# Kernel tuning notes

Measured on AMD Instinct MI355X. Metric: run time of the kernel, lower is better.

Reference implementation:

```python
import jax, jax.numpy as jnp
import numpy as np
from jax import lax

D_MODEL, D_INNER, D_STATE, DT_RANK, K = 96, 192, 16, 6, 4
B_, H_, W_ = 8, 64, 64

def setup_inputs() -> dict:
    key = jax.random.key(0)
    ks = jax.random.split(key, 12)
    return {
        "x": jax.random.normal(ks[0], (B_, H_, W_, D_MODEL), jnp.float32),
        "in_proj_w": jax.random.normal(ks[1], (2 * D_INNER, D_MODEL), jnp.float32) * 0.05,
        "conv_w": jax.random.normal(ks[2], (D_INNER, 1, 3, 3), jnp.float32) * 0.1,
        "conv_b": jax.random.normal(ks[3], (D_INNER,), jnp.float32) * 0.01,
        "x_proj_w": jax.random.normal(ks[4], (K, DT_RANK + 2 * D_STATE, D_INNER), jnp.float32) * 0.05,
        "dt_proj_w": jax.random.normal(ks[5], (K, D_INNER, DT_RANK), jnp.float32) * 0.1,
        "dt_proj_b": jax.random.normal(ks[6], (K, D_INNER), jnp.float32) * 0.1,
        "A_logs": jax.random.uniform(ks[7], (K * D_INNER, D_STATE), jnp.float32, 0.0, 2.0),
        "Ds": jnp.ones((K * D_INNER,), jnp.float32),
        "ln_g": jnp.ones((D_INNER,), jnp.float32),
        "ln_b": jnp.zeros((D_INNER,), jnp.float32),
        "out_proj_w": jax.random.normal(ks[8], (D_MODEL, D_INNER), jnp.float32) * 0.05,
    }

def _selective_scan(xs, delta, A, Bs, Cs, Dk):
    # xs/delta: (B,K,D,L); A: (K,D,N); Bs/Cs: (B,K,N,L); Dk: (K,D)
    u_t = xs.transpose(3, 0, 1, 2)      # (L,B,K,D)
    d_t = delta.transpose(3, 0, 1, 2)   # (L,B,K,D)
    B_t = Bs.transpose(3, 0, 1, 2)      # (L,B,K,N)
    C_t = Cs.transpose(3, 0, 1, 2)      # (L,B,K,N)
    b = xs.shape[0]
    h0 = jnp.zeros((b, K, D_INNER, D_STATE), xs.dtype)
    def step(h, inp):
        ul, dl, Bl, Cl = inp
        dA = jnp.exp(dl[..., None] * A)                 # (B,K,D,N)
        h = dA * h + (dl * ul)[..., None] * Bl[:, :, None, :]
        y = jnp.einsum('bkdn,bkn->bkd', h, Cl)
        return h, y
    _, ys = lax.scan(step, h0, (u_t, d_t, B_t, C_t))
    y = ys.transpose(1, 2, 3, 0)                         # (B,K,D,L)
    return y + xs * Dk[None, :, :, None]

def reference(x, in_proj_w, conv_w, conv_b, x_proj_w, dt_proj_w, dt_proj_b,
              A_logs, Ds, ln_g, ln_b, out_proj_w):
    B, H, W, C = x.shape
    L = H * W
    xz = jnp.einsum('bhwc,ec->bhwe', x, in_proj_w)       # (B,H,W,2*D_inner)
    xc, z = jnp.split(xz, 2, axis=-1)
    xc = xc.transpose(0, 3, 1, 2)                        # (B,D,H,W)
    xc = lax.conv_general_dilated(xc, conv_w, (1, 1), 'SAME',
                                  dimension_numbers=('NCHW', 'OIHW', 'NCHW'),
                                  feature_group_count=D_INNER)
    xa = jax.nn.silu(xc + conv_b[None, :, None, None])
    x_flat = xa.reshape(B, D_INNER, L)
    x_wh = xa.transpose(0, 1, 3, 2).reshape(B, D_INNER, L)
    x_hwwh = jnp.stack([x_flat, x_wh], axis=1)           # (B,2,D,L)
    xs = jnp.concatenate([x_hwwh, jnp.flip(x_hwwh, -1)], axis=1)  # (B,4,D,L)
    x_dbl = jnp.einsum('bkdl,kcd->bkcl', xs, x_proj_w)
    dts = x_dbl[:, :, :DT_RANK]
    Bs = x_dbl[:, :, DT_RANK:DT_RANK + D_STATE]
    Cs = x_dbl[:, :, DT_RANK + D_STATE:]
    dts = jnp.einsum('bkrl,kdr->bkdl', dts, dt_proj_w)
    delta = jax.nn.softplus(dts + dt_proj_b[None, :, :, None])
    A = -jnp.exp(A_logs).reshape(K, D_INNER, D_STATE)
    Dk = Ds.reshape(K, D_INNER)
    out_y = _selective_scan(xs, delta, A, Bs, Cs, Dk)    # (B,4,D,L)
    y1 = out_y[:, 0]
    inv = jnp.flip(out_y[:, 2:4], -1)
    y2 = inv[:, 0]
    y3 = out_y[:, 1].reshape(B, D_INNER, W, H).transpose(0, 1, 3, 2).reshape(B, D_INNER, L)
    y4 = inv[:, 1].reshape(B, D_INNER, W, H).transpose(0, 1, 3, 2).reshape(B, D_INNER, L)
    y = (y1 + y2 + y3 + y4).transpose(0, 2, 1).reshape(B, H, W, D_INNER)
    mu = y.mean(-1, keepdims=True)
    var = ((y - mu) ** 2).mean(-1, keepdims=True)
    y = (y - mu) * lax.rsqrt(var + 1e-5) * ln_g + ln_b
    y = y * jax.nn.silu(z)
    return jnp.einsum('bhwd,cd->bhwc', y, out_proj_w)
```

## Files before the change

kernel.cpp:

```cpp
#include <hip/hip_runtime.h>

#define B_  8
#define L_  4096
#define DI  192
#define LOG2E 1.44269504f
#define LN2F  0.69314718f

#if __has_builtin(__builtin_amdgcn_exp2f)
#define EXP2(x) __builtin_amdgcn_exp2f(x)
#else
#define EXP2(x) __expf((x)*LN2F)
#endif

__global__ __launch_bounds__(256) void k_inproj(
    const float* __restrict__ x, const float* __restrict__ w,
    float* __restrict__ xc, float* __restrict__ z)
{
  __shared__ float As[96*68];
  __shared__ float Ws[96*68];
  const int t  = threadIdx.x;
  const int m0 = blockIdx.x * 64;
  const int n0 = blockIdx.y * 64;
  for (int i = t; i < 64*24; i += 256) {
    const int row = i / 24, q = (i % 24) * 4;
    const float4 v = *(const float4*)&x[(size_t)(m0+row)*96 + q];
    As[(q+0)*68 + row] = v.x; As[(q+1)*68 + row] = v.y;
    As[(q+2)*68 + row] = v.z; As[(q+3)*68 + row] = v.w;
  }
  for (int i = t; i < 64*24; i += 256) {
    const int row = i / 24, q = (i % 24) * 4;
    const float4 v = *(const float4*)&w[(size_t)(n0+row)*96 + q];
    Ws[(q+0)*68 + row] = v.x; Ws[(q+1)*68 + row] = v.y;
    Ws[(q+2)*68 + row] = v.z; Ws[(q+3)*68 + row] = v.w;
  }
  __syncthreads();
  const int tx = t & 15, ty = t >> 4;
  float acc[4][4] = {};
#pragma unroll 4
  for (int kk = 0; kk < 96; ++kk) {
    const float4 a4 = *(const float4*)&As[kk*68 + ty*4];
    const float4 b4 = *(const float4*)&Ws[kk*68 + tx*4];
    const float a[4] = {a4.x, a4.y, a4.z, a4.w};
    const float b[4] = {b4.x, b4.y, b4.z, b4.w};
#pragma unroll
    for (int i = 0; i < 4; ++i)
#pragma unroll
      for (int j = 0; j < 4; ++j) acc[i][j] = fmaf(a[i], b[j], acc[i][j]);
  }
#pragma unroll
  for (int i = 0; i < 4; ++i) {
    const int row = m0 + ty*4 + i;
#pragma unroll
    for (int j = 0; j < 4; ++j) {
      const int col = n0 + tx*4 + j;
      if (col < DI) xc[(size_t)row*DI + col]      = acc[i][j];
      else          z [(size_t)row*DI + col - DI] = acc[i][j];
    }
  }
}

__global__ __launch_bounds__(192) void k_conv(
    const float* __restrict__ xc, const float* __restrict__ cw,
    const float* __restrict__ cb, float* __restrict__ xa)
{
  const int bi = blockIdx.x;
  const int d  = threadIdx.x;
  const int b = bi >> 12, s = bi & 4095;
  const int h = s >> 6, w = s & 63;
  float wreg[9];
#pragma unroll
  for (int i = 0; i < 9; ++i) wreg[i] = cw[d*9 + i];
  float acc = cb[d];
#pragma unroll
  for (int ky = 0; ky < 3; ++ky) {
    const int hy = h + ky - 1;
    if (hy < 0 || hy > 63) continue;
#pragma unroll
    for (int kx = 0; kx < 3; ++kx) {
      const int wx = w + kx - 1;
      if (wx < 0 || wx > 63) continue;
      acc = fmaf(xc[(size_t)((b<<12) + (hy<<6) + wx)*DI + d], wreg[ky*3+kx], acc);
    }
  }
  const float sig = 1.f / (1.f + __expf(-acc));
  xa[(size_t)bi*DI + d] = acc * sig;
}

#define WSL(c,q) ((c)*36 + ((((q) ^ (((c)>>2)&7)) & 7) << 2))
__global__ __launch_bounds__(256) void k_xproj(
    const float* __restrict__ xa, const float* __restrict__ xw,
    float* __restrict__ proj)
{
  __shared__ float V[64*196];
  __shared__ float W[152*36];
  const int t  = threadIdx.x;
  const int s0 = blockIdx.x * 64;
  for (int i = t; i < 64*48; i += 256) {
    const int row = i / 48;
    const int q   = (i % 48) * 4;
    *(float4*)&V[row*196 + q] = *(const float4*)&xa[(size_t)(s0+row)*192 + q];
  }
  const int tx = t & 15;
  const int ty = t >> 4;
  const int c0 = tx * 10;
  float acc[4][10] = {};
#pragma unroll 1
  for (int p = 0; p < 6; ++p) {
    __syncthreads();
    for (int i = t; i < 152*8; i += 256) {
      const int c = i >> 3, q = i & 7;
      *(float4*)&W[WSL(c,q)] = *(const float4*)&xw[(size_t)c*192 + p*32 + q*4];
    }
    __syncthreads();
#pragma unroll
    for (int rs = 0; rs < 8; ++rs) {
      const int r0 = p*32 + rs*4;
      float av[4][4];
#pragma unroll
      for (int m = 0; m < 4; ++m) {
        const float4 a4 = *(const float4*)&V[(ty*4+m)*196 + r0];
        av[m][0]=a4.x; av[m][1]=a4.y; av[m][2]=a4.z; av[m][3]=a4.w;
      }
      float wr[10][4];
#pragma unroll
      for (int j = 0; j < 10; ++j) {
        const int cg = (c0 + j < 152) ? c0 + j : 151;
        const float4 w4 = *(const float4*)&W[WSL(cg,rs)];
        wr[j][0]=w4.x; wr[j][1]=w4.y; wr[j][2]=w4.z; wr[j][3]=w4.w;
      }
#pragma unroll
      for (int i = 0; i < 4; ++i)
#pragma unroll
        for (int m = 0; m < 4; ++m)
#pragma unroll
          for (int j = 0; j < 10; ++j)
            acc[m][j] = fmaf(av[m][i], wr[j][i], acc[m][j]);
    }
  }
  __syncthreads();
  float* Csm = V;
#pragma unroll
  for (int m = 0; m < 4; ++m)
#pragma unroll
    for (int j = 0; j < 10; ++j)
      if (c0 + j < 152) Csm[(ty*4+m)*162 + c0 + j] = acc[m][j];
  __syncthreads();
  const int b = s0 >> 12;
  const int sbase = s0 & 4095;
#pragma unroll 1
  for (int k = 0; k < 4; ++k) {
    float* op = proj + ((size_t)((b<<2)+k)*L_ + sbase)*40;
#pragma unroll
    for (int it = 0; it < 10; ++it) {
      const int f = it*256 + t;
      const int s = f / 40, c = f - s*40;
      op[f] = (c < 38) ? Csm[s*162 + k*38 + c] : 0.f;
    }
  }
}

template<int NC>
__global__ __launch_bounds__(192) void k_scan1(
    const float* __restrict__ xa, const float* __restrict__ proj,
    const float* __restrict__ alog, const float* __restrict__ dtw,
    const float* __restrict__ dtb,
    float* __restrict__ P, float* __restrict__ Hl)
{
  constexpr int CL = L_ / NC;
  const int blk = blockIdx.x;
  const int c = blk % NC, k = (blk / NC) & 3, b = blk / (NC*4);
  const int d = threadIdx.x;
  const int kd = k*DI + d;
  const int rev = (k >> 1) & 1, sw = k & 1;
  float A2[16], dw[6];
#pragma unroll
  for (int n = 0; n < 16; ++n) A2[n] = -__expf(alog[kd*16 + n]) * LOG2E;
#pragma unroll
  for (int r = 0; r < 6; ++r) dw[r] = dtw[kd*6 + r];
  const float db = dtb[kd];
  float h[16];
#pragma unroll
  for (int n = 0; n < 16; ++n) h[n] = 0.f;
  float Sd = 0.f;
  const int l0 = c * CL;
  const int l2_0 = rev ? 4095 - l0 : l0;
  const int sbase = sw ? (((l2_0 & 63) << 6) | (l2_0 >> 6)) : l2_0;
  const int stp = sw ? (rev ? -64 : 64) : (rev ? -1 : 1);
  const float* up = xa + ((size_t)(b << 12) + sbase)*DI + d;
  const char* pr8 = (const char*)(proj + ((((size_t)((b<<2)+k)) << 12) + sbase)*40);
  const ptrdiff_t ustep = (ptrdiff_t)stp * DI;
  const ptrdiff_t pstepB = (ptrdiff_t)stp * 160;
#pragma unroll 2
  for (int t = 0; t < CL; ++t) {
    const float u = *up;
    const float4 q0 = *(const float4*)(pr8 +  0);
    const float4 q1 = *(const float4*)(pr8 + 16);
    const float4 q2 = *(const float4*)(pr8 + 32);
    const float4 q3 = *(const float4*)(pr8 + 48);
    const float4 q4 = *(const float4*)(pr8 + 64);
    const float4 q5 = *(const float4*)(pr8 + 80);
    float xdt = db;
    xdt = fmaf(dw[0], q0.x, xdt); xdt = fmaf(dw[1], q0.y, xdt);
    xdt = fmaf(dw[2], q0.z, xdt); xdt = fmaf(dw[3], q0.w, xdt);
    xdt = fmaf(dw[4], q1.x, xdt); xdt = fmaf(dw[5], q1.y, xdt);
    const float delta = (xdt > 20.f) ? xdt
                       : LN2F * __log2f(1.f + EXP2(xdt * LOG2E));
    Sd += delta;
    const float du = delta * u;
    const float Bv[16] = {q1.z,q1.w,q2.x,q2.y,q2.z,q2.w,q3.x,q3.y,
                          q3.z,q3.w,q4.x,q4.y,q4.z,q4.w,q5.x,q5.y};
#pragma unroll
    for (int n = 0; n < 16; ++n) {
      const float dA = EXP2(delta * A2[n]);
      h[n] = fmaf(dA, h[n], du * Bv[n]);
    }
    up += ustep; pr8 += pstepB;
  }
  const size_t base = (size_t)blk * 16 * DI + d;
#pragma unroll
  for (int n = 0; n < 16; ++n) {
    P[base + n*DI]  = EXP2(A2[n] * Sd);
    Hl[base + n*DI] = h[n];
  }
}

template<int NC, bool ZERO>
__global__ __launch_bounds__(256) void k_scan2(
    const float* P, const float* __restrict__ Hl, float* hin,
    float* __restrict__ ycomb)
{
  const int tid = blockIdx.x * 256 + threadIdx.x;
  if (ZERO)
    for (size_t i = tid; i < (size_t)B_*L_*DI; i += 98304) ycomb[i] = 0.f;
  const int d  = tid % DI;
  const int n  = (tid / DI) & 15;
  const int bk = tid / (DI*16);
  float h = 0.f;
  for (int cc = 0; cc < NC; ++cc) {
    const size_t idx = ((size_t)(bk*NC + cc)*16 + n)*DI + d;
    const float pv = P[idx];
    const float hl = Hl[idx];
    hin[idx] = h;
    h = fmaf(pv, h, hl);
  }
}

template<int NC>
__global__ __launch_bounds__(192) void k_scan3f(
    const float* __restrict__ xa, const float* __restrict__ proj,
    const float* __restrict__ alog, const float* __restrict__ dtw,
    const float* __restrict__ dtb, const float* __restrict__ Dv,
    const float* __restrict__ hin,
    float* __restrict__ y0, float* __restrict__ y1,
    float* __restrict__ y2, float* __restrict__ y3)
{
  constexpr int CL = L_ / NC;
  const int blk = blockIdx.x;
  const int c = blk % NC, k = (blk / NC) & 3, b = blk / (NC*4);
  const int d = threadIdx.x;
  const int kd = k*DI + d;
  const int rev = (k >> 1) & 1, sw = k & 1;
  float A2[16], dw[6];
#pragma unroll
  for (int n = 0; n < 16; ++n) A2[n] = -__expf(alog[kd*16 + n]) * LOG2E;
#pragma unroll
  for (int r = 0; r < 6; ++r) dw[r] = dtw[kd*6 + r];
  const float db = dtb[kd];
  const float Dd = Dv[kd];
  float h[16];
  const size_t base = (size_t)blk * 16 * DI + d;
#pragma unroll
  for (int n = 0; n < 16; ++n) h[n] = hin[base + n*DI];
  const int l0 = c * CL;
  const int l2_0 = rev ? 4095 - l0 : l0;
  const int sbase = sw ? (((l2_0 & 63) << 6) | (l2_0 >> 6)) : l2_0;
  const int stp = sw ? (rev ? -64 : 64) : (rev ? -1 : 1);
  const float* up = xa + ((size_t)(b << 12) + sbase)*DI + d;
  const char* pr8 = (const char*)(proj + ((((size_t)((b<<2)+k)) << 12) + sbase)*40);
  const ptrdiff_t ustep = (ptrdiff_t)stp * DI;
  const ptrdiff_t pstepB = (ptrdiff_t)stp * 160;
  float* yb = (k == 0) ? y0 : (k == 1) ? y1 : (k == 2) ? y2 : y3;
  float* yp = yb + ((size_t)(b << 12) + l2_0)*DI + d;
  const ptrdiff_t ystep = (ptrdiff_t)(rev ? -1 : 1) * DI;
#pragma unroll 2
  for (int t = 0; t < CL; ++t) {
    const float u = *up;
    const float4 q0 = *(const float4*)(pr8 +   0);
    const float4 q1 = *(const float4*)(pr8 +  16);
    const float4 q2 = *(const float4*)(pr8 +  32);
    const float4 q3 = *(const float4*)(pr8 +  48);
    const float4 q4 = *(const float4*)(pr8 +  64);
    const float4 q5 = *(const float4*)(pr8 +  80);
    const float4 q6 = *(const float4*)(pr8 +  96);
    const float4 q7 = *(const float4*)(pr8 + 112);
    const float4 q8 = *(const float4*)(pr8 + 128);
    const float4 q9 = *(const float4*)(pr8 + 144);
    float xdt = db;
    xdt = fmaf(dw[0], q0.x, xdt); xdt = fmaf(dw[1], q0.y, xdt);
    xdt = fmaf(dw[2], q0.z, xdt); xdt = fmaf(dw[3], q0.w, xdt);
    xdt = fmaf(dw[4], q1.x, xdt); xdt = fmaf(dw[5], q1.y, xdt);
    const float delta = (xdt > 20.f) ? xdt
                       : LN2F * __log2f(1.f + EXP2(xdt * LOG2E));
    const float du = delta * u;
    const float Bv[16] = {q1.z,q1.w,q2.x,q2.y,q2.z,q2.w,q3.x,q3.y,
                          q3.z,q3.w,q4.x,q4.y,q4.z,q4.w,q5.x,q5.y};
    const float Cv[16] = {q5.z,q5.w,q6.x,q6.y,q6.z,q6.w,q7.x,q7.y,
                          q7.z,q7.w,q8.x,q8.y,q8.z,q8.w,q9.x,q9.y};
    float y = 0.f;
#pragma unroll
    for (int n = 0; n < 16; ++n) {
      const float dA = EXP2(delta * A2[n]);
      h[n] = fmaf(dA, h[n], du * Bv[n]);
      y = fmaf(h[n], Cv[n], y);
    }
    y = fmaf(u, Dd, y);
    *yp = y;
    yp += ystep; up += ustep; pr8 += pstepB;
  }
}

template<int NC>
__global__ __launch_bounds__(192) void k_scan3a(
    const float* __restrict__ xa, const float* __restrict__ proj,
    const float* __restrict__ alog, const float* __restrict__ dtw,
    const float* __restrict__ dtb, const float* __restrict__ Dv,
    const float* __restrict__ hin, float* __restrict__ ycomb)
{
  constexpr int CL = L_ / NC;
  const int blk = blockIdx.x;
  const int c = blk % NC, k = (blk / NC) & 3, b = blk / (NC*4);
  const int d = threadIdx.x;
  const int kd = k*DI + d;
  const int rev = (k >> 1) & 1, sw = k & 1;
  float A2[16], dw[6];
#pragma unroll
  for (int n = 0; n < 16; ++n) A2[n] = -__expf(alog[kd*16 + n]) * LOG2E;
#pragma unroll
  for (int r = 0; r < 6; ++r) dw[r] = dtw[kd*6 + r];
  const float db = dtb[kd];
  const float Dd = Dv[kd];
  float h[16];
  const size_t base = (size_t)blk * 16 * DI + d;
#pragma unroll
  for (int n = 0; n < 16; ++n) h[n] = hin[base + n*DI];
  const int l0 = c * CL;
  const float* xab = xa + (size_t)(b << 12)*DI + d;
  const float* pb  = proj + (((size_t)((b<<2)+k)) << 12)*40;
#pragma unroll 2
  for (int t = 0; t < CL; ++t) {
    const int l = l0 + t;
    const int l2 = rev ? 4095 - l : l;
    const int s  = sw ? (((l2 & 63) << 6) | (l2 >> 6)) : l2;
    const float u = xab[(size_t)s*DI];
    const float* pp = pb + (size_t)s*40;
    float xdt = db;
#pragma unroll
    for (int r = 0; r < 6; ++r) xdt = fmaf(dw[r], pp[r], xdt);
    const float delta = (xdt > 20.f) ? xdt : __logf(1.f + __expf(xdt));
    const float du = delta * u;
    float y = 0.f;
#pragma unroll
    for (int n = 0; n < 16; ++n) {
      const float dA = EXP2(delta * A2[n]);
      h[n] = fmaf(dA, h[n], du * pp[6+n]);
      y = fmaf(h[n], pp[22+n], y);
    }
    y = fmaf(u, Dd, y);
    atomicAdd(&ycomb[(size_t)((b<<12) + s)*DI + d], y);
  }
}

template<int MODE>
__global__ __launch_bounds__(256) void k_final(
    const float* __restrict__ y0, const float* __restrict__ y1,
    const float* __restrict__ y2, const float* __restrict__ y3,
    const float* __restrict__ zb,
    const float* __restrict__ lng, const float* __restrict__ lnb,
    const float* __restrict__ ow, float* __restrict__ out)
{
  __shared__ float yt[192*68];
  __shared__ float W2[96*36];
  const int t = threadIdx.x;
  const int lane = t & 63, wv = t >> 6;
  const int g0 = blockIdx.x * 64;
  for (int si = 0; si < 16; ++si) {
    const int sl = wv*16 + si;
    const int g  = g0 + sl;
    const int s  = g & 4095;
    const size_t r13 = (size_t)(g & ~4095) | (((s & 63) << 6) | (s >> 6));
    float v[3]; float sum = 0.f, sq = 0.f;
#pragma unroll
    for (int j = 0; j < 3; ++j) {
      const int ch = lane*3 + j;
      float vv = y0[(size_t)g*DI + ch];
      if (MODE == 0)
        vv += y2[(size_t)g*DI + ch] + y1[r13*DI + ch] + y3[r13*DI + ch];
      v[j] = vv;
      sum += vv; sq = fmaf(vv, vv, sq);
    }
#pragma unroll
    for (int o = 1; o < 64; o <<= 1) { sum += __shfl_xor(sum, o); sq += __shfl_xor(sq, o); }
    const float mu = sum * (1.f/192.f);
    const float rs = rsqrtf(sq*(1.f/192.f) - mu*mu + 1e-5f);
#pragma unroll
    for (int j = 0; j < 3; ++j) {
      const int ch = lane*3 + j;
      const float zv = zb[(size_t)g*DI + ch];
      const float sz = zv / (1.f + __expf(-zv));
      yt[ch*68 + sl] = ((v[j]-mu)*rs*lng[ch] + lnb[ch]) * sz;
    }
  }
  __syncthreads();
  const int tx = t & 15, ty = t >> 4;
  const int c0 = tx*6;
  float acc[4][6] = {};
#pragma unroll 1
  for (int p = 0; p < 6; ++p) {
    if (p) __syncthreads();
    for (int i = t; i < 96*8; i += 256) {
      const int c = i >> 3, q = i & 7;
      *(float4*)&W2[WSL(c,q)] = *(const float4*)&ow[(size_t)c*192 + p*32 + q*4];
    }
    __syncthreads();
#pragma unroll
    for (int rs = 0; rs < 8; ++rs) {
      const int k4 = p*32 + rs*4;
      float4 bw[6];
#pragma unroll
      for (int j = 0; j < 6; ++j) bw[j] = *(const float4*)&W2[WSL(c0+j, rs)];
#pragma unroll
      for (int i4 = 0; i4 < 4; ++i4) {
        const float4 a4 = *(const float4*)&yt[(k4+i4)*68 + ty*4];
        const float av[4] = {a4.x, a4.y, a4.z, a4.w};
        const float bv[6] = {
          i4==0?bw[0].x:i4==1?bw[0].y:i4==2?bw[0].z:bw[0].w,
          i4==0?bw[1].x:i4==1?bw[1].y:i4==2?bw[1].z:bw[1].w,
          i4==0?bw[2].x:i4==1?bw[2].y:i4==2?bw[2].z:bw[2].w,
          i4==0?bw[3].x:i4==1?bw[3].y:i4==2?bw[3].z:bw[3].w,
          i4==0?bw[4].x:i4==1?bw[4].y:i4==2?bw[4].z:bw[4].w,
          i4==0?bw[5].x:i4==1?bw[5].y:i4==2?bw[5].z:bw[5].w };
#pragma unroll
        for (int i = 0; i < 4; ++i)
#pragma unroll
          for (int j = 0; j < 6; ++j) acc[i][j] = fmaf(av[i], bv[j], acc[i][j]);
      }
    }
  }
#pragma unroll
  for (int i = 0; i < 4; ++i) {
    const size_t row = (size_t)(g0 + ty*4 + i)*96 + c0;
#pragma unroll
    for (int j = 0; j < 6; ++j) out[row + j] = acc[i][j];
  }
}

extern "C" void kernel_launch(void* const* d_in, const int* in_sizes, int n_in,
                              void* d_out, int out_size, void* d_ws, size_t ws_size,
                              hipStream_t stream)
{
  (void)in_sizes; (void)n_in; (void)out_size;
  const float* x    = (const float*)d_in[0];
  const float* ipw  = (const float*)d_in[1];
  const float* cw   = (const float*)d_in[2];
  const float* cb   = (const float*)d_in[3];
  const float* xpw  = (const float*)d_in[4];
  const float* dpw  = (const float*)d_in[5];
  const float* dpb  = (const float*)d_in[6];
  const float* alog = (const float*)d_in[7];
  const float* Dv   = (const float*)d_in[8];
  const float* lng  = (const float*)d_in[9];
  const float* lnb  = (const float*)d_in[10];
  const float* opw  = (const float*)d_in[11];
  float* out = (float*)d_out;

  float* ws    = (float*)d_ws;
  float* xc    = ws;
  float* zbuf  = ws + 6291456;
  float* xa    = ws + 12582912;
  float* proj  = ws + 18874368;
  float* after = ws + 24117248;
  const size_t YSZ = 6291456;

  k_inproj<<<dim3(512, 6), 256, 0, stream>>>(x, ipw, xc, zbuf);
  k_conv  <<<32768, 192, 0, stream>>>(xc, cw, cb, xa);
  k_xproj <<<512, 256, 0, stream>>>(xa, xpw, proj);

  const size_t needF128 = (24117248ull + 2ull*98304*128 + YSZ) * 4;
  const size_t needF64  = (24117248ull + 2ull*98304*64  + 2*YSZ) * 4;
  const size_t needB    = 30408704ull * 4;

  if (ws_size >= needF128) {
    constexpr int NC = 128;
    float* Pb  = after;
    float* Hlb = after + (size_t)98304*NC;
    float* y1  = Hlb;
    float* y2  = Hlb + YSZ;
    float* y3  = after + 2ull*98304*NC;
    k_scan1<NC><<<8*4*NC, 192, 0, stream>>>(xa, proj, alog, dpw, dpb, Pb, Hlb);
    k_scan2<NC,false><<<384, 256, 0, stream>>>(Pb, Hlb, Pb, nullptr);
    k_scan3f<NC><<<8*4*NC, 192, 0, stream>>>(xa, proj, alog, dpw, dpb, Dv, Pb, xc, y1, y2, y3);
    k_final<0><<<512, 256, 0, stream>>>(xc, y1, y2, y3, zbuf, lng, lnb, opw, out);
  } else if (ws_size >= needF64) {
    constexpr int NC = 64;
    float* Pb  = after;
    float* Hlb = after + (size_t)98304*NC;
    float* y1  = Hlb;
    float* y2  = after + 2ull*98304*NC;
    float* y3  = y2 + YSZ;
    k_scan1<NC><<<8*4*NC, 192, 0, stream>>>(xa, proj, alog, dpw, dpb, Pb, Hlb);
    k_scan2<NC,false><<<384, 256, 0, stream>>>(Pb, Hlb, Pb, nullptr);
    k_scan3f<NC><<<8*4*NC, 192, 0, stream>>>(xa, proj, alog, dpw, dpb, Dv, Pb, xc, y1, y2, y3);
    k_final<0><<<512, 256, 0, stream>>>(xc, y1, y2, y3, zbuf, lng, lnb, opw, out);
  } else if (ws_size >= needB) {
    constexpr int NC = 32;
    float* Pb  = after;
    float* Hlb = after + (size_t)98304*NC;
    k_scan1<NC><<<8*4*NC, 192, 0, stream>>>(xa, proj, alog, dpw, dpb, Pb, Hlb);
    k_scan2<NC,true><<<384, 256, 0, stream>>>(Pb, Hlb, Pb, xc);
    k_scan3a<NC><<<8*4*NC, 192, 0, stream>>>(xa, proj, alog, dpw, dpb, Dv, Pb, xc);
    k_final<1><<<512, 256, 0, stream>>>(xc, nullptr, nullptr, nullptr, zbuf, lng, lnb, opw, out);
  } else {
    constexpr int NC = 16;
    float* Pb  = after;
    float* Hlb = after + (size_t)98304*NC;
    k_scan1<NC><<<8*4*NC, 192, 0, stream>>>(xa, proj, alog, dpw, dpb, Pb, Hlb);
    k_scan2<NC,true><<<384, 256, 0, stream>>>(Pb, Hlb, Pb, xc);
    k_scan3a<NC><<<8*4*NC, 192, 0, stream>>>(xa, proj, alog, dpw, dpb, Dv, Pb, xc);
    k_final<1><<<512, 256, 0, stream>>>(xc, nullptr, nullptr, nullptr, zbuf, lng, lnb, opw, out);
  }
}
```

Baseline: 372.4 us.

## Slide conv window along width and drop the NC=128 scan path

The depthwise 3x3 conv now has each block process 16 consecutive width positions of one row. A register-held 3x3 window slides along the row, so each step loads only the three new column values instead of all nine, and the block count shrinks. The NC=128 chunked scan branch is also removed, so when workspace allows, the 64-chunk path runs instead. Dropping that branch changes scan parallelism and may cost scan throughput, since fewer chunks means longer sequential chunks.

Result: faster. 337.0 us (-9.5%).

```diff
diff --git a/kernel.cpp b/kernel.cpp
--- a/kernel.cpp
+++ b/kernel.cpp
@@ -63,27 +63,42 @@
     const float* __restrict__ xc, const float* __restrict__ cw,
     const float* __restrict__ cb, float* __restrict__ xa)
 {
-  const int bi = blockIdx.x;
+  const int blk = blockIdx.x;
+  const int wg = blk & 3, h = (blk >> 2) & 63, b = blk >> 8;
   const int d  = threadIdx.x;
-  const int b = bi >> 12, s = bi & 4095;
-  const int h = s >> 6, w = s & 63;
   float wreg[9];
 #pragma unroll
   for (int i = 0; i < 9; ++i) wreg[i] = cw[d*9 + i];
-  float acc = cb[d];
-#pragma unroll
-  for (int ky = 0; ky < 3; ++ky) {
-    const int hy = h + ky - 1;
-    if (hy < 0 || hy > 63) continue;
-#pragma unroll
-    for (int kx = 0; kx < 3; ++kx) {
-      const int wx = w + kx - 1;
-      if (wx < 0 || wx > 63) continue;
-      acc = fmaf(xc[(size_t)((b<<12) + (hy<<6) + wx)*DI + d], wreg[ky*3+kx], acc);
-    }
-  }
-  const float sig = 1.f / (1.f + __expf(-acc));
-  xa[(size_t)bi*DI + d] = acc * sig;
+  const float bias = cb[d];
+  const float* base = xc + ((size_t)(b) << 12)*DI + d;
+  const int w0 = wg * 16;
+  const bool hm = (h > 0), hp = (h < 63);
+  auto LD = [&](int hh, int ww, bool ok) -> float {
+    return ok ? base[(size_t)((hh << 6) + ww)*DI] : 0.f;
+  };
+  float a0 = LD(h-1, w0-1, hm && w0 > 0);
+  float a1 = LD(h,   w0-1, w0 > 0);
+  float a2 = LD(h+1, w0-1, hp && w0 > 0);
+  float b0 = LD(h-1, w0, hm);
+  float b1 = LD(h,   w0, true);
+  float b2 = LD(h+1, w0, hp);
+  float* op = xa + ((size_t)((b << 12) + (h << 6) + w0))*DI + d;
+#pragma unroll 4
+  for (int w = w0; w < w0 + 16; ++w) {
+    const bool wp = (w < 63);
+    const float c0 = LD(h-1, w+1, hm && wp);
+    const float c1 = LD(h,   w+1, wp);
+    const float c2 = LD(h+1, w+1, hp && wp);
+    float acc = bias;
+    acc = fmaf(a0, wreg[0], acc); acc = fmaf(b0, wreg[1], acc); acc = fmaf(c0, wreg[2], acc);
+    acc = fmaf(a1, wreg[3], acc); acc = fmaf(b1, wreg[4], acc); acc = fmaf(c1, wreg[5], acc);
+    acc = fmaf(a2, wreg[6], acc); acc = fmaf(b2, wreg[7], acc); acc = fmaf(c2, wreg[8], acc);
+    const float sig = 1.f / (1.f + __expf(-acc));
+    *op = acc * sig;
+    op += DI;
+    a0 = b0; a1 = b1; a2 = b2;
+    b0 = c0; b1 = c1; b2 = c2;
+  }
 }
 
 #define WSL(c,q) ((c)*36 + ((((q) ^ (((c)>>2)&7)) & 7) << 2))
@@ -482,25 +497,13 @@
   const size_t YSZ = 6291456;
 
   k_inproj<<<dim3(512, 6), 256, 0, stream>>>(x, ipw, xc, zbuf);
-  k_conv  <<<32768, 192, 0, stream>>>(xc, cw, cb, xa);
+  k_conv  <<<2048, 192, 0, stream>>>(xc, cw, cb, xa);
   k_xproj <<<512, 256, 0, stream>>>(xa, xpw, proj);
 
-  const size_t needF128 = (24117248ull + 2ull*98304*128 + YSZ) * 4;
   const size_t needF64  = (24117248ull + 2ull*98304*64  + 2*YSZ) * 4;
   const size_t needB    = 30408704ull * 4;
 
-  if (ws_size >= needF128) {
-    constexpr int NC = 128;
-    float* Pb  = after;
-    float* Hlb = after + (size_t)98304*NC;
-    float* y1  = Hlb;
-    float* y2  = Hlb + YSZ;
-    float* y3  = after + 2ull*98304*NC;
-    k_scan1<NC><<<8*4*NC, 192, 0, stream>>>(xa, proj, alog, dpw, dpb, Pb, Hlb);
-    k_scan2<NC,false><<<384, 256, 0, stream>>>(Pb, Hlb, Pb, nullptr);
-    k_scan3f<NC><<<8*4*NC, 192, 0, stream>>>(xa, proj, alog, dpw, dpb, Dv, Pb, xc, y1, y2, y3);
-    k_final<0><<<512, 256, 0, stream>>>(xc, y1, y2, y3, zbuf, lng, lnb, opw, out);
-  } else if (ws_size >= needF64) {
+  if (ws_size >= needF64) {
     constexpr int NC = 64;
     float* Pb  = after;
     float* Hlb = after + (size_t)98304*NC;
```
